# Performance work log

Measured on AMD Instinct MI355X. Metric: run time of the kernel, lower is better.

The kernel has to match this reference:

```python
import jax, jax.numpy as jnp
import numpy as np
from itertools import combinations

B, F, E, V = 4096, 39, 40, 1000000
BN_EPS = 1e-3  # tf.layers.batch_normalization default epsilon


def setup_inputs() -> dict:
    key = jax.random.key(0)
    k_in, k_w, k_v, k_e = jax.random.split(key, 4)
    inputs = jax.random.randint(k_in, (B, F), 0, V, dtype=jnp.int64)
    # generate_pairs(range(F)): cols = first elements, rows = second elements
    pairs = np.array(list(combinations(range(F), 2)), dtype=np.int64)  # [741, 2]
    cols = jnp.asarray(pairs[:, 0])
    rows = jnp.asarray(pairs[:, 1])
    w = jax.random.normal(k_w, (V,), dtype=jnp.float32) * 0.01
    v = jax.random.normal(k_v, (V, E), dtype=jnp.float32) * (1.0 / np.sqrt(E))
    b = jnp.zeros((), dtype=jnp.float32)
    # edge weights init ~ uniform(weight_base - 1e-3, weight_base + 1e-3)
    edge_weights = jax.random.uniform(k_e, (pairs.shape[0],), dtype=jnp.float32,
                                      minval=0.599, maxval=0.601)
    return {"inputs": inputs, "rows": rows, "cols": cols,
            "w": w, "v": v, "b": b, "edge_weights": edge_weights}


def reference(inputs, rows, cols, w, v, b, edge_weights):
    # Embedding lookups
    xw = w[inputs]                      # [B, F]  first-order weights
    xv = v[inputs]                      # [B, F, E] second-order embeddings
    l = jnp.sum(xw, axis=1)             # [B] linear term

    # Pairwise FM interactions: gather field pairs, multiply, reduce over embed
    left = xv[:, rows]                  # [B, P, E]
    right = xv[:, cols]                 # [B, P, E]
    level_2 = jnp.sum(left * right, axis=-1)  # [B, P]

    # BatchNorm (training mode, scale=False, center=False): batch stats per pair
    mean = jnp.mean(level_2, axis=0)
    var = jnp.var(level_2, axis=0)      # biased variance, as in TF BN
    level_2 = (level_2 - mean) * jax.lax.rsqrt(var + BN_EPS)

    # Edge-weight (architecture) mask
    level_2 = level_2 * edge_weights[None, :]

    fm_out = jnp.sum(level_2, axis=-1)  # [B]
    logits = l + fm_out + b             # [B]
    return logits
```

## Files before the change

kernel.cpp:

```cpp
#include <hip/hip_runtime.h>

#define NF 39
#define NE 40
#define NB 4096
#define NSLOT 1536
#define NBLK 512
#define SPW 2
#define SPB 8
#define K2_BLOCKS 48
#define EPS 1.0e-3f

typedef __attribute__((ext_vector_type(8))) short short8;
typedef __attribute__((ext_vector_type(4))) float floatx4;

__device__ __forceinline__ unsigned int f2bf(float f) {
    unsigned int b = __float_as_uint(f);
    b += 0x7FFFu + ((b >> 16) & 1u);
    return b >> 16;
}

__device__ __forceinline__ float bf2f(unsigned int u) {
    return __uint_as_float(u << 16);
}

__device__ __forceinline__ short8 pack8(float4 a, float4 b) {
    union { unsigned int u[4]; short8 s; } o;
    o.u[0] = f2bf(a.x) | (f2bf(a.y) << 16);
    o.u[1] = f2bf(a.z) | (f2bf(a.w) << 16);
    o.u[2] = f2bf(b.x) | (f2bf(b.y) << 16);
    o.u[3] = f2bf(b.z) | (f2bf(b.w) << 16);
    return o.s;
}

__device__ __forceinline__ void load_frags(
    const int* __restrict__ ip, const float* __restrict__ v,
    int rbase, int ehalf, short8 F0[3], short8 F1[3])
{
    const float4 zero4 = {0.f, 0.f, 0.f, 0.f};
#pragma unroll
    for (int I = 0; I < 3; ++I) {
        const int r = rbase + 16 * I;
        const bool vr = (r < NF);
        const int id = vr ? ip[r] : 0;
        const float* vrow = v + (size_t)id * NE;
        const float4 a  = vr ? *reinterpret_cast<const float4*>(vrow + ehalf * 8)     : zero4;
        const float4 bq = vr ? *reinterpret_cast<const float4*>(vrow + ehalf * 8 + 4) : zero4;
        F0[I] = pack8(a, bq);
        const bool v1 = vr && (ehalf == 0);
        const float4 c_ = v1 ? *reinterpret_cast<const float4*>(vrow + 32) : zero4;
        const float4 d_ = v1 ? *reinterpret_cast<const float4*>(vrow + 36) : zero4;
        F1[I] = pack8(c_, d_);
    }
}

__device__ __forceinline__ void gram_mfma(const short8 F0[3], const short8 F1[3], floatx4 acc[6])
{
    acc[0] = __builtin_amdgcn_mfma_f32_16x16x32_bf16(F0[0], F0[0], acc[0], 0, 0, 0);
    acc[1] = __builtin_amdgcn_mfma_f32_16x16x32_bf16(F0[0], F0[1], acc[1], 0, 0, 0);
    acc[2] = __builtin_amdgcn_mfma_f32_16x16x32_bf16(F0[0], F0[2], acc[2], 0, 0, 0);
    acc[3] = __builtin_amdgcn_mfma_f32_16x16x32_bf16(F0[1], F0[1], acc[3], 0, 0, 0);
    acc[4] = __builtin_amdgcn_mfma_f32_16x16x32_bf16(F0[1], F0[2], acc[4], 0, 0, 0);
    acc[5] = __builtin_amdgcn_mfma_f32_16x16x32_bf16(F0[2], F0[2], acc[5], 0, 0, 0);
    acc[0] = __builtin_amdgcn_mfma_f32_16x16x32_bf16(F1[0], F1[0], acc[0], 0, 0, 0);
    acc[1] = __builtin_amdgcn_mfma_f32_16x16x32_bf16(F1[0], F1[1], acc[1], 0, 0, 0);
    acc[2] = __builtin_amdgcn_mfma_f32_16x16x32_bf16(F1[0], F1[2], acc[2], 0, 0, 0);
    acc[3] = __builtin_amdgcn_mfma_f32_16x16x32_bf16(F1[1], F1[1], acc[3], 0, 0, 0);
    acc[4] = __builtin_amdgcn_mfma_f32_16x16x32_bf16(F1[1], F1[2], acc[4], 0, 0, 0);
    acc[5] = __builtin_amdgcn_mfma_f32_16x16x32_bf16(F1[2], F1[2], acc[5], 0, 0, 0);
}

__global__ __launch_bounds__(256) void fm_k1(
    const int* __restrict__ inputs, const float* __restrict__ w,
    const float* __restrict__ v, unsigned short* __restrict__ Gb,
    float* __restrict__ lsum, unsigned int* __restrict__ partial)
{
    __shared__ float red[4 * 2 * NSLOT];
    const int t = threadIdx.x, wid = t >> 6, lane = t & 63;
    const int rbase = lane & 15, ehalf = lane >> 4;
    const int b0 = blockIdx.x * SPB;

    floatx4 sum[6] = {}, sq[6] = {};
#pragma unroll
    for (int s = 0; s < SPW; ++s) {
        const int smp = b0 + wid * SPW + s;
        const int* ip = inputs + (size_t)smp * NF;
        short8 F0[3], F1[3];
        load_frags(ip, v, rbase, ehalf, F0, F1);

        float wv = (lane < NF) ? w[ip[lane]] : 0.0f;
#pragma unroll
        for (int o = 32; o > 0; o >>= 1) wv += __shfl_down(wv, o, 64);
        if (lane == 0) lsum[smp] = wv;

        floatx4 acc[6] = {};
        gram_mfma(F0, F1, acc);

        unsigned short* gr = Gb + (size_t)smp * NSLOT;
#pragma unroll
        for (int tl = 0; tl < 6; ++tl) {
            uint2 pk;
            pk.x = f2bf(acc[tl][0]) | (f2bf(acc[tl][1]) << 16);
            pk.y = f2bf(acc[tl][2]) | (f2bf(acc[tl][3]) << 16);
            *reinterpret_cast<uint2*>(gr + tl * 256 + lane * 4) = pk;
            sum[tl] += acc[tl];
            sq[tl]  += acc[tl] * acc[tl];
        }
    }

    float* rw = &red[wid * 2 * NSLOT];
#pragma unroll
    for (int tl = 0; tl < 6; ++tl) {
        *reinterpret_cast<floatx4*>(rw + tl * 256 + lane * 4)         = sum[tl];
        *reinterpret_cast<floatx4*>(rw + NSLOT + tl * 256 + lane * 4) = sq[tl];
    }
    __syncthreads();
    unsigned int* po = partial + (size_t)blockIdx.x * NSLOT;
    for (int j = t; j < NSLOT; j += 256) {
        const float s = red[j] + red[2 * NSLOT + j] + red[4 * NSLOT + j] + red[6 * NSLOT + j];
        const float q = red[NSLOT + j] + red[3 * NSLOT + j] + red[5 * NSLOT + j] + red[7 * NSLOT + j];
        po[j] = (f2bf(s) << 16) | f2bf(q);
    }
}

__global__ __launch_bounds__(256) void fm_k2(
    const unsigned int* __restrict__ partial, const float* __restrict__ ew,
    float* __restrict__ meanArr, float* __restrict__ scaleArr)
{
    const int t = threadIdx.x;
    const int slotL = t & 31, rg = t >> 5;
    const int slot0 = blockIdx.x * 32;
    float s1 = 0.f, s2 = 0.f;
#pragma unroll 8
    for (int r = 0; r < 64; ++r) {
        const unsigned int u = partial[(size_t)(rg * 64 + r) * NSLOT + slot0 + slotL];
        s1 += __uint_as_float(u & 0xFFFF0000u);
        s2 += __uint_as_float(u << 16);
    }
    __shared__ float r1[8][32], r2[8][32];
    r1[rg][slotL] = s1;
    r2[rg][slotL] = s2;
    __syncthreads();
    if (t < 32) {
        float a = 0.f, b = 0.f;
#pragma unroll
        for (int g = 0; g < 8; ++g) { a += r1[g][t]; b += r2[g][t]; }
        const int slot = slot0 + t;
        const float m   = a * (1.0f / NB);
        const float var = b * (1.0f / NB) - m * m;
        const int tile = slot >> 8;
        const int l    = (slot & 255) >> 2;
        const int q    = slot & 3;
        const int TI[6] = {0, 0, 0, 1, 1, 2};
        const int TJ[6] = {0, 1, 2, 1, 2, 2};
        const int gi = 16 * TI[tile] + ((l >> 4) << 2) + q;
        const int gj = 16 * TJ[tile] + (l & 15);
        float scl = 0.0f;
        if (gi < gj && gj < NF) {
            const int p = 38 * gi - (gi * (gi - 1)) / 2 + (gj - gi - 1);
            scl = ew[p] * rsqrtf(var + EPS);
        }
        meanArr[slot]  = m;
        scaleArr[slot] = scl;
    }
}

__global__ __launch_bounds__(256) void fm_k3(
    const unsigned short* __restrict__ Gb, const float* __restrict__ lsum,
    const float* __restrict__ meanArr, const float* __restrict__ scaleArr,
    const float* __restrict__ bias, float* __restrict__ out)
{
    const int t = threadIdx.x, wid = t >> 6, lane = t & 63;
    const int b0 = blockIdx.x * SPB;

    floatx4 mf[6], sf[6];
#pragma unroll
    for (int tl = 0; tl < 6; ++tl) {
        mf[tl] = *reinterpret_cast<const floatx4*>(meanArr  + tl * 256 + lane * 4);
        sf[tl] = *reinterpret_cast<const floatx4*>(scaleArr + tl * 256 + lane * 4);
    }
    const float bs = bias[0];

#pragma unroll
    for (int s = 0; s < SPW; ++s) {
        const int smp = b0 + wid * SPW + s;
        const unsigned short* gr = Gb + (size_t)smp * NSLOT;
        float tot = (lane == 0) ? lsum[smp] : 0.0f;
#pragma unroll
        for (int tl = 0; tl < 6; ++tl) {
            const uint2 pk = *reinterpret_cast<const uint2*>(gr + tl * 256 + lane * 4);
            tot += (bf2f(pk.x & 0xFFFFu) - mf[tl][0]) * sf[tl][0];
            tot += (bf2f(pk.x >> 16)     - mf[tl][1]) * sf[tl][1];
            tot += (bf2f(pk.y & 0xFFFFu) - mf[tl][2]) * sf[tl][2];
            tot += (bf2f(pk.y >> 16)     - mf[tl][3]) * sf[tl][3];
        }
#pragma unroll
        for (int o = 32; o > 0; o >>= 1) tot += __shfl_down(tot, o, 64);
        if (lane == 0) out[smp] = tot + bs;
    }
}

extern "C" void kernel_launch(void* const* d_in, const int* in_sizes, int n_in,
                              void* d_out, int out_size, void* d_ws, size_t ws_size,
                              hipStream_t stream)
{
    const int*   inputs = (const int*)  d_in[0];
    const float* w      = (const float*)d_in[3];
    const float* v      = (const float*)d_in[4];
    const float* bias   = (const float*)d_in[5];
    const float* ew     = (const float*)d_in[6];
    float*       out    = (float*)      d_out;

    unsigned short* Gb = (unsigned short*)d_ws;
    unsigned int* partial = (unsigned int*)(Gb + (size_t)NB * NSLOT);
    float* meanA   = (float*)(partial + (size_t)NBLK * NSLOT);
    float* scaleA  = meanA + NSLOT;
    float* lsum    = scaleA + NSLOT;

    fm_k1<<<NBLK,      256, 0, stream>>>(inputs, w, v, Gb, lsum, partial);
    fm_k2<<<K2_BLOCKS, 256, 0, stream>>>(partial, ew, meanA, scaleA);
    fm_k3<<<NBLK,      256, 0, stream>>>(Gb, lsum, meanA, scaleA, bias, out);
}
```

Baseline: 27.91 us.

## Compact Gram intermediate to the 741 valid pairs via shared-memory scatter

Kernel 1 now scatters only the valid upper-triangle pair products into a dense per-sample shared buffer, then writes it out as 768 bf16 values instead of the padded 1536-slot tile layout. Kernel 2 emits mean/scale in the same dense pair order, and kernel 3 reads the halved intermediate with coalesced 32-bit loads. This cuts global write/read traffic of the intermediate in half, at the cost of scattered LDS stores and two extra block-wide barriers per sample in kernel 1.

```diff
diff --git a/kernel.cpp b/kernel.cpp
--- a/kernel.cpp
+++ b/kernel.cpp
@@ -3,6 +3,8 @@
 #define NF 39
 #define NE 40
 #define NB 4096
+#define NP 741
+#define NDW 384
 #define NSLOT 1536
 #define NBLK 512
 #define SPW 2
@@ -71,13 +73,18 @@
 
 __global__ __launch_bounds__(256) void fm_k1(
     const int* __restrict__ inputs, const float* __restrict__ w,
-    const float* __restrict__ v, unsigned short* __restrict__ Gb,
+    const float* __restrict__ v, unsigned int* __restrict__ Gd,
     float* __restrict__ lsum, unsigned int* __restrict__ partial)
 {
-    __shared__ float red[4 * 2 * NSLOT];
+    __shared__ union {
+        unsigned short dense[4][2 * NDW];
+        float red[4 * 2 * NSLOT];
+    } sm;
     const int t = threadIdx.x, wid = t >> 6, lane = t & 63;
     const int rbase = lane & 15, ehalf = lane >> 4;
     const int b0 = blockIdx.x * SPB;
+    const int TI[6] = {0, 0, 0, 1, 1, 2};
+    const int TJ[6] = {0, 1, 2, 1, 2, 2};
 
     floatx4 sum[6] = {}, sq[6] = {};
 #pragma unroll
@@ -94,20 +101,34 @@
 
         floatx4 acc[6] = {};
         gram_mfma(F0, F1, acc);
-
-        unsigned short* gr = Gb + (size_t)smp * NSLOT;
 #pragma unroll
         for (int tl = 0; tl < 6; ++tl) {
-            uint2 pk;
-            pk.x = f2bf(acc[tl][0]) | (f2bf(acc[tl][1]) << 16);
-            pk.y = f2bf(acc[tl][2]) | (f2bf(acc[tl][3]) << 16);
-            *reinterpret_cast<uint2*>(gr + tl * 256 + lane * 4) = pk;
             sum[tl] += acc[tl];
             sq[tl]  += acc[tl] * acc[tl];
         }
-    }
-
-    float* rw = &red[wid * 2 * NSLOT];
+
+        unsigned short* dw = sm.dense[wid];
+        if (lane < 2 * NDW - NP) dw[NP + lane] = 0;
+#pragma unroll
+        for (int tl = 0; tl < 6; ++tl)
+#pragma unroll
+            for (int q = 0; q < 4; ++q) {
+                const int gi = 16 * TI[tl] + 4 * ehalf + q;
+                const int gj = 16 * TJ[tl] + rbase;
+                if (gi < gj && gj < NF) {
+                    const int p = 38 * gi - (gi * (gi - 1)) / 2 + (gj - gi - 1);
+                    dw[p] = (unsigned short)f2bf(acc[tl][q]);
+                }
+            }
+        __syncthreads();
+        const unsigned int* dwu = reinterpret_cast<const unsigned int*>(dw);
+        unsigned int* go = Gd + (size_t)smp * NDW;
+#pragma unroll
+        for (int k = 0; k < 6; ++k) go[lane + 64 * k] = dwu[lane + 64 * k];
+        __syncthreads();
+    }
+
+    float* rw = &sm.red[wid * 2 * NSLOT];
 #pragma unroll
     for (int tl = 0; tl < 6; ++tl) {
         *reinterpret_cast<floatx4*>(rw + tl * 256 + lane * 4)         = sum[tl];
@@ -116,19 +137,23 @@
     __syncthreads();
     unsigned int* po = partial + (size_t)blockIdx.x * NSLOT;
     for (int j = t; j < NSLOT; j += 256) {
-        const float s = red[j] + red[2 * NSLOT + j] + red[4 * NSLOT + j] + red[6 * NSLOT + j];
-        const float q = red[NSLOT + j] + red[3 * NSLOT + j] + red[5 * NSLOT + j] + red[7 * NSLOT + j];
+        const float s = sm.red[j] + sm.red[2 * NSLOT + j] + sm.red[4 * NSLOT + j] + sm.red[6 * NSLOT + j];
+        const float q = sm.red[NSLOT + j] + sm.red[3 * NSLOT + j] + sm.red[5 * NSLOT + j] + sm.red[7 * NSLOT + j];
         po[j] = (f2bf(s) << 16) | f2bf(q);
     }
 }
 
 __global__ __launch_bounds__(256) void fm_k2(
     const unsigned int* __restrict__ partial, const float* __restrict__ ew,
-    float* __restrict__ meanArr, float* __restrict__ scaleArr)
+    float* __restrict__ meanD, float* __restrict__ scaleD)
 {
     const int t = threadIdx.x;
     const int slotL = t & 31, rg = t >> 5;
     const int slot0 = blockIdx.x * 32;
+    if (blockIdx.x == 0 && t >= 64 && t < 64 + (2 * NDW - NP)) {
+        meanD[NP + t - 64]  = 0.0f;
+        scaleD[NP + t - 64] = 0.0f;
+    }
     float s1 = 0.f, s2 = 0.f;
 #pragma unroll 8
     for (int r = 0; r < 64; ++r) {
@@ -154,44 +179,40 @@
         const int TJ[6] = {0, 1, 2, 1, 2, 2};
         const int gi = 16 * TI[tile] + ((l >> 4) << 2) + q;
         const int gj = 16 * TJ[tile] + (l & 15);
-        float scl = 0.0f;
         if (gi < gj && gj < NF) {
             const int p = 38 * gi - (gi * (gi - 1)) / 2 + (gj - gi - 1);
-            scl = ew[p] * rsqrtf(var + EPS);
+            meanD[p]  = m;
+            scaleD[p] = ew[p] * rsqrtf(var + EPS);
         }
-        meanArr[slot]  = m;
-        scaleArr[slot] = scl;
     }
 }
 
 __global__ __launch_bounds__(256) void fm_k3(
-    const unsigned short* __restrict__ Gb, const float* __restrict__ lsum,
-    const float* __restrict__ meanArr, const float* __restrict__ scaleArr,
+    const unsigned int* __restrict__ Gd, const float* __restrict__ lsum,
+    const float* __restrict__ meanD, const float* __restrict__ scaleD,
     const float* __restrict__ bias, float* __restrict__ out)
 {
     const int t = threadIdx.x, wid = t >> 6, lane = t & 63;
     const int b0 = blockIdx.x * SPB;
 
-    floatx4 mf[6], sf[6];
-#pragma unroll
-    for (int tl = 0; tl < 6; ++tl) {
-        mf[tl] = *reinterpret_cast<const floatx4*>(meanArr  + tl * 256 + lane * 4);
-        sf[tl] = *reinterpret_cast<const floatx4*>(scaleArr + tl * 256 + lane * 4);
+    float2 mf[6], sf[6];
+#pragma unroll
+    for (int k = 0; k < 6; ++k) {
+        mf[k] = *reinterpret_cast<const float2*>(meanD  + 2 * (lane + 64 * k));
+        sf[k] = *reinterpret_cast<const float2*>(scaleD + 2 * (lane + 64 * k));
     }
     const float bs = bias[0];
 
 #pragma unroll
     for (int s = 0; s < SPW; ++s) {
         const int smp = b0 + wid * SPW + s;
-        const unsigned short* gr = Gb + (size_t)smp * NSLOT;
+        const unsigned int* gr = Gd + (size_t)smp * NDW;
         float tot = (lane == 0) ? lsum[smp] : 0.0f;
 #pragma unroll
-        for (int tl = 0; tl < 6; ++tl) {
-            const uint2 pk = *reinterpret_cast<const uint2*>(gr + tl * 256 + lane * 4);
-            tot += (bf2f(pk.x & 0xFFFFu) - mf[tl][0]) * sf[tl][0];
-            tot += (bf2f(pk.x >> 16)     - mf[tl][1]) * sf[tl][1];
-            tot += (bf2f(pk.y & 0xFFFFu) - mf[tl][2]) * sf[tl][2];
-            tot += (bf2f(pk.y >> 16)     - mf[tl][3]) * sf[tl][3];
+        for (int k = 0; k < 6; ++k) {
+            const unsigned int u = gr[lane + 64 * k];
+            tot += (bf2f(u & 0xFFFFu) - mf[k].x) * sf[k].x;
+            tot += (bf2f(u >> 16)     - mf[k].y) * sf[k].y;
         }
 #pragma unroll
         for (int o = 32; o > 0; o >>= 1) tot += __shfl_down(tot, o, 64);
@@ -210,13 +231,13 @@
     const float* ew     = (const float*)d_in[6];
     float*       out    = (float*)      d_out;
 
-    unsigned short* Gb = (unsigned short*)d_ws;
-    unsigned int* partial = (unsigned int*)(Gb + (size_t)NB * NSLOT);
-    float* meanA   = (float*)(partial + (size_t)NBLK * NSLOT);
-    float* scaleA  = meanA + NSLOT;
-    float* lsum    = scaleA + NSLOT;
-
-    fm_k1<<<NBLK,      256, 0, stream>>>(inputs, w, v, Gb, lsum, partial);
-    fm_k2<<<K2_BLOCKS, 256, 0, stream>>>(partial, ew, meanA, scaleA);
-    fm_k3<<<NBLK,      256, 0, stream>>>(Gb, lsum, meanA, scaleA, bias, out);
-}
+    unsigned int* Gd      = (unsigned int*)d_ws;
+    unsigned int* partial = Gd + (size_t)NB * NDW;
+    float* meanD  = (float*)(partial + (size_t)NBLK * NSLOT);
+    float* scaleD = meanD + 2 * NDW;
+    float* lsum   = scaleD + 2 * NDW;
+
+    fm_k1<<<NBLK,      256, 0, stream>>>(inputs, w, v, Gd, lsum, partial);
+    fm_k2<<<K2_BLOCKS, 256, 0, stream>>>(partial, ew, meanD, scaleD);
+    fm_k3<<<NBLK,      256, 0, stream>>>(Gd, lsum, meanD, scaleD, bias, out);
+}
```

Result: no change. 28.34 us (+1.5%).

## Fuse BN statistics finalize into first kernel via last-blocks atomic counter

Applied to the files above, without the earlier changes.

Removes the separate statistics-reduction kernel. Each block of the first kernel takes a ticket from a global atomic counter, and the last 48 blocks to arrive spin until every block has finished, then reduce the partial sums into mean and scale. This removes one kernel launch and its boundary gap, but adds a memset launch, atomics and spin-waiting. It also relies on the last-ranked blocks being resident, which holds because they are already running when they take their ticket.

```diff
diff --git a/kernel.cpp b/kernel.cpp
--- a/kernel.cpp
+++ b/kernel.cpp
@@ -7,7 +7,7 @@
 #define NBLK 512
 #define SPW 2
 #define SPB 8
-#define K2_BLOCKS 48
+#define FIN_BLOCKS 48
 #define EPS 1.0e-3f
 
 typedef __attribute__((ext_vector_type(8))) short short8;
@@ -71,10 +71,13 @@
 
 __global__ __launch_bounds__(256) void fm_k1(
     const int* __restrict__ inputs, const float* __restrict__ w,
-    const float* __restrict__ v, unsigned short* __restrict__ Gb,
-    float* __restrict__ lsum, unsigned int* __restrict__ partial)
+    const float* __restrict__ v, const float* __restrict__ ew,
+    unsigned short* __restrict__ Gb, float* __restrict__ lsum,
+    unsigned int* __restrict__ partial, float* __restrict__ meanArr,
+    float* __restrict__ scaleArr, unsigned int* __restrict__ cnt)
 {
     __shared__ float red[4 * 2 * NSLOT];
+    __shared__ unsigned int rank_sm;
     const int t = threadIdx.x, wid = t >> 6, lane = t & 63;
     const int rbase = lane & 15, ehalf = lane >> 4;
     const int b0 = blockIdx.x * SPB;
@@ -120,15 +123,24 @@
         const float q = red[NSLOT + j] + red[3 * NSLOT + j] + red[5 * NSLOT + j] + red[7 * NSLOT + j];
         po[j] = (f2bf(s) << 16) | f2bf(q);
     }
-}
-
-__global__ __launch_bounds__(256) void fm_k2(
-    const unsigned int* __restrict__ partial, const float* __restrict__ ew,
-    float* __restrict__ meanArr, float* __restrict__ scaleArr)
-{
-    const int t = threadIdx.x;
+
+    __threadfence();
+    __syncthreads();
+    if (t == 0) rank_sm = __hip_atomic_fetch_add(&cnt[0], 1u, __ATOMIC_ACQ_REL, __HIP_MEMORY_SCOPE_AGENT);
+    __syncthreads();
+    const unsigned int rank = rank_sm;
+    if (rank < NBLK - FIN_BLOCKS) return;
+
+    const int fb = (int)rank - (NBLK - FIN_BLOCKS);
+    if (t == 0) {
+        while (__hip_atomic_load(&cnt[0], __ATOMIC_ACQUIRE, __HIP_MEMORY_SCOPE_AGENT) < NBLK)
+            __builtin_amdgcn_s_sleep(2);
+    }
+    __syncthreads();
+    __threadfence();
+
     const int slotL = t & 31, rg = t >> 5;
-    const int slot0 = blockIdx.x * 32;
+    const int slot0 = fb * 32;
     float s1 = 0.f, s2 = 0.f;
 #pragma unroll 8
     for (int r = 0; r < 64; ++r) {
@@ -136,14 +148,15 @@
         s1 += __uint_as_float(u & 0xFFFF0000u);
         s2 += __uint_as_float(u << 16);
     }
-    __shared__ float r1[8][32], r2[8][32];
-    r1[rg][slotL] = s1;
-    r2[rg][slotL] = s2;
+    float* r1 = red;
+    float* r2 = red + 256;
+    r1[rg * 32 + slotL] = s1;
+    r2[rg * 32 + slotL] = s2;
     __syncthreads();
     if (t < 32) {
         float a = 0.f, b = 0.f;
 #pragma unroll
-        for (int g = 0; g < 8; ++g) { a += r1[g][t]; b += r2[g][t]; }
+        for (int g = 0; g < 8; ++g) { a += r1[g * 32 + t]; b += r2[g * 32 + t]; }
         const int slot = slot0 + t;
         const float m   = a * (1.0f / NB);
         const float var = b * (1.0f / NB) - m * m;
@@ -215,8 +228,9 @@
     float* meanA   = (float*)(partial + (size_t)NBLK * NSLOT);
     float* scaleA  = meanA + NSLOT;
     float* lsum    = scaleA + NSLOT;
-
-    fm_k1<<<NBLK,      256, 0, stream>>>(inputs, w, v, Gb, lsum, partial);
-    fm_k2<<<K2_BLOCKS, 256, 0, stream>>>(partial, ew, meanA, scaleA);
-    fm_k3<<<NBLK,      256, 0, stream>>>(Gb, lsum, meanA, scaleA, bias, out);
-}
+    unsigned int* cnt = (unsigned int*)(lsum + NB);
+
+    hipMemsetAsync(cnt, 0, sizeof(unsigned int), stream);
+    fm_k1<<<NBLK, 256, 0, stream>>>(inputs, w, v, ew, Gb, lsum, partial, meanA, scaleA, cnt);
+    fm_k3<<<NBLK, 256, 0, stream>>>(Gb, lsum, meanA, scaleA, bias, out);
+}
```

After: 95.96 us. 3.44x slower.
